# Kernel tuning notes

Hardware: AMD Instinct MI355X
Metric: run time of the kernel (lower is better)

The kernel has to match this reference:

```python
import jax, jax.numpy as jnp
import numpy as np

D, H, E = 1024, 4096, 8


def setup_inputs() -> dict:
    key = jax.random.key(0)
    ks = jax.random.split(key, 5)
    x = jax.random.normal(ks[0], (4, 2048, D), dtype=jnp.float32)
    gate_w = jax.random.normal(ks[1], (D, E), dtype=jnp.float32) * 0.02
    gate_b = jnp.zeros((E,), dtype=jnp.float32)
    w1 = jax.random.normal(ks[2], (E, D, H), dtype=jnp.float32) * 0.02
    b1 = jnp.zeros((E, H), dtype=jnp.float32)
    w2 = jax.random.normal(ks[3], (E, H, D), dtype=jnp.float32) * 0.02
    b2 = jnp.zeros((E, D), dtype=jnp.float32)
    return {"x": x, "gate_w": gate_w, "gate_b": gate_b,
            "w1": w1, "b1": b1, "w2": w2, "b2": b2, "top_k": 2}


def reference(x, gate_w, gate_b, w1, b1, w2, b2, top_k):
    orig_shape = x.shape
    xt = x.reshape(-1, x.shape[-1])                 # [T, D]
    logits = xt @ gate_w + gate_b                   # [T, E]
    probs = jax.nn.softmax(logits, axis=-1)
    topk_v, topk_i = jax.lax.top_k(probs, top_k)    # [T, k]
    T, n_exp = probs.shape
    # dense combine weights: zero for non-selected experts (same math as
    # sorted dispatch + weighted scatter-add in the original)
    comb = jnp.zeros((T, n_exp), xt.dtype).at[
        jnp.arange(T)[:, None], topk_i].set(topk_v)  # [T, E]

    def step(acc, params):
        W1, B1, W2, B2, g = params                  # g: [T]
        h = jax.nn.gelu(xt @ W1 + B1, approximate=False)  # exact erf GELU
        return acc + g[:, None] * (h @ W2 + B2), None

    out, _ = jax.lax.scan(step, jnp.zeros_like(xt),
                          (w1, b1, w2, b2, comb.T))
    return out.reshape(orig_shape)
```

## Files before the change

kernel.cpp:

```cpp
#include <hip/hip_runtime.h>
#include <hip/hip_bf16.h>


#define T_TOK 8192
#define DDIM  1024
#define HDIM  4096
#define NEXP  8

typedef __attribute__((ext_vector_type(8))) short sv8;
typedef __attribute__((ext_vector_type(4))) float fv4;

__device__ __forceinline__ float gelu_erf(float v) {
    return 0.5f * v * (1.0f + erff(v * 0.70710678118654752f));
}

__device__ __forceinline__ unsigned short f2bfbits(float f) {
    unsigned int x; __builtin_memcpy(&x, &f, 4);
    x += 0x7fffu + ((x >> 16) & 1u);
    return (unsigned short)(x >> 16);
}

__device__ __forceinline__ void split2(float f, short& h, short& l) {
    unsigned int x; __builtin_memcpy(&x, &f, 4);
    unsigned int hr = x + (0x7fffu + ((x >> 16) & 1u));
    unsigned int hbits = hr & 0xffff0000u;
    float hf; __builtin_memcpy(&hf, &hbits, 4);
    h = (short)(hr >> 16);
    l = (short)f2bfbits(f - hf);
}

__global__ __launch_bounds__(256) void zero_kernel(float* __restrict__ out,
                                                   int n, int* __restrict__ counts) {
    int i = blockIdx.x * 256 + threadIdx.x;
    if (i < n) out[i] = 0.0f;
    if (blockIdx.x == 0 && threadIdx.x < 16) counts[threadIdx.x] = 0;
}

__global__ __launch_bounds__(256) void gate_kernel(
    const float* __restrict__ x, const float* __restrict__ gw,
    const float* __restrict__ gb, int* __restrict__ counts,
    int* __restrict__ tok_idx, float* __restrict__ tok_gate) {
    const int token = blockIdx.x * 4 + (threadIdx.x >> 6);
    const int lane  = threadIdx.x & 63;
    const float* xr = x + (size_t)token * DDIM;

    float acc[8] = {0.f, 0.f, 0.f, 0.f, 0.f, 0.f, 0.f, 0.f};
    for (int d = lane; d < DDIM; d += 64) {
        const float xv = xr[d];
        const float4 g0 = *(const float4*)(gw + d * NEXP);
        const float4 g1 = *(const float4*)(gw + d * NEXP + 4);
        acc[0] = fmaf(xv, g0.x, acc[0]); acc[1] = fmaf(xv, g0.y, acc[1]);
        acc[2] = fmaf(xv, g0.z, acc[2]); acc[3] = fmaf(xv, g0.w, acc[3]);
        acc[4] = fmaf(xv, g1.x, acc[4]); acc[5] = fmaf(xv, g1.y, acc[5]);
        acc[6] = fmaf(xv, g1.z, acc[6]); acc[7] = fmaf(xv, g1.w, acc[7]);
    }
#pragma unroll
    for (int e = 0; e < 8; ++e)
        for (int off = 32; off > 0; off >>= 1)
            acc[e] += __shfl_down(acc[e], off);

    if (lane == 0) {
#pragma unroll
        for (int e = 0; e < 8; ++e) acc[e] += gb[e];
        float m = acc[0];
#pragma unroll
        for (int e = 1; e < 8; ++e) m = fmaxf(m, acc[e]);
        float p[8], s = 0.f;
#pragma unroll
        for (int e = 0; e < 8; ++e) { p[e] = expf(acc[e] - m); s += p[e]; }
        const float inv = 1.0f / s;
#pragma unroll
        for (int e = 0; e < 8; ++e) p[e] *= inv;
        int i1 = 0;
#pragma unroll
        for (int e = 1; e < 8; ++e) if (p[e] > p[i1]) i1 = e;
        int i2 = (i1 == 0) ? 1 : 0;
#pragma unroll
        for (int e = 0; e < 8; ++e) if (e != i1 && p[e] > p[i2]) i2 = e;

        int pos1 = atomicAdd(&counts[i1], 1);
        tok_idx[i1 * T_TOK + pos1]  = token;
        tok_gate[i1 * T_TOK + pos1] = p[i1];
        int pos2 = atomicAdd(&counts[i2], 1);
        tok_idx[i2 * T_TOK + pos2]  = token;
        tok_gate[i2 * T_TOK + pos2] = p[i2];
    }
}

__global__ void offs_kernel(const int* __restrict__ counts, int* __restrict__ offs) {
    if (threadIdx.x == 0 && blockIdx.x == 0) {
        int s = 0;
#pragma unroll
        for (int e = 0; e < NEXP; ++e) { offs[e] = s; s += counts[e]; }
        offs[NEXP] = s;
    }
}

__global__ __launch_bounds__(256) void ffn1_mfma(
    const float* __restrict__ x, const float* __restrict__ w1,
    const float* __restrict__ b1, const int* __restrict__ counts,
    const int* __restrict__ offs, const int* __restrict__ tok_idx,
    unsigned short* __restrict__ Hbuf) {
    const int e   = blockIdx.z;
    const int cnt = counts[e];
    const int m0  = blockIdx.y * 128;
    if (m0 >= cnt) return;
    const int n0  = blockIdx.x * 128;

    __shared__ __align__(16) short Ah[128][32], Al[128][32];
    __shared__ __align__(16) short Bh[128][32], Bl[128][32];
    __shared__ int stok[128];

    const int tid  = threadIdx.x;
    const int lane = tid & 63;
    const int wv   = tid >> 6;
    const int wr   = wv >> 1, wc = wv & 1;
    const int r16  = lane & 15, g4 = lane >> 4;

    if (tid < 128) stok[tid] = tok_idx[e * T_TOK + min(m0 + tid, cnt - 1)];
    __syncthreads();

    const float* W = w1 + (size_t)e * DDIM * HDIM;

    fv4 acc[4][4];
    const fv4 z4 = {0.f, 0.f, 0.f, 0.f};
#pragma unroll
    for (int i = 0; i < 4; ++i)
#pragma unroll
        for (int j = 0; j < 4; ++j) acc[i][j] = z4;

    for (int k0 = 0; k0 < DDIM; k0 += 32) {
#pragma unroll
        for (int h = 0; h < 2; ++h) {
            const int c   = tid + h * 256;
            const int row = c >> 2, kc = c & 3;
            const float* src = x + (size_t)stok[row] * DDIM + k0 + kc * 8;
            const float4 f0 = *(const float4*)src;
            const float4 f1 = *(const float4*)(src + 4);
            const float f[8] = {f0.x, f0.y, f0.z, f0.w, f1.x, f1.y, f1.z, f1.w};
            sv8 hv, lv;
#pragma unroll
            for (int i = 0; i < 8; ++i) { short hh, ll; split2(f[i], hh, ll); hv[i] = hh; lv[i] = ll; }
            *(sv8*)&Ah[row][kc * 8] = hv;
            *(sv8*)&Al[row][kc * 8] = lv;
        }
#pragma unroll
        for (int h = 0; h < 2; ++h) {
            const int c  = tid + h * 256;
            const int nn = c >> 2, kc = c & 3;
            float f[8];
#pragma unroll
            for (int i = 0; i < 8; ++i)
                f[i] = W[(size_t)(k0 + kc * 8 + i) * HDIM + n0 + nn];
            sv8 hv, lv;
#pragma unroll
            for (int i = 0; i < 8; ++i) { short hh, ll; split2(f[i], hh, ll); hv[i] = hh; lv[i] = ll; }
            *(sv8*)&Bh[nn][kc * 8] = hv;
            *(sv8*)&Bl[nn][kc * 8] = lv;
        }
        __syncthreads();

        sv8 a_h[4], a_l[4], b_h[4], b_l[4];
#pragma unroll
        for (int m = 0; m < 4; ++m) {
            const int row = wr * 64 + m * 16 + r16;
            a_h[m] = *(const sv8*)&Ah[row][g4 * 8];
            a_l[m] = *(const sv8*)&Al[row][g4 * 8];
        }
#pragma unroll
        for (int n = 0; n < 4; ++n) {
            const int col = wc * 64 + n * 16 + r16;
            b_h[n] = *(const sv8*)&Bh[col][g4 * 8];
            b_l[n] = *(const sv8*)&Bl[col][g4 * 8];
        }
#pragma unroll
        for (int m = 0; m < 4; ++m)
#pragma unroll
            for (int n = 0; n < 4; ++n) {
                acc[m][n] = __builtin_amdgcn_mfma_f32_16x16x32_bf16(a_h[m], b_h[n], acc[m][n], 0, 0, 0);
                acc[m][n] = __builtin_amdgcn_mfma_f32_16x16x32_bf16(a_h[m], b_l[n], acc[m][n], 0, 0, 0);
                acc[m][n] = __builtin_amdgcn_mfma_f32_16x16x32_bf16(a_l[m], b_h[n], acc[m][n], 0, 0, 0);
            }
        __syncthreads();
    }

    const int hbase = offs[e] + m0;
#pragma unroll
    for (int n = 0; n < 4; ++n) {
        const int colg = n0 + wc * 64 + n * 16 + r16;
        const float bias = b1[e * HDIM + colg];
#pragma unroll
        for (int m = 0; m < 4; ++m) {
#pragma unroll
            for (int r = 0; r < 4; ++r) {
                const int rowl = wr * 64 + m * 16 + g4 * 4 + r;
                if (m0 + rowl < cnt) {
                    const float v = gelu_erf(acc[m][n][r] + bias);
                    Hbuf[(size_t)(hbase + rowl) * HDIM + colg] = f2bfbits(v);
                }
            }
        }
    }
}

__global__ __launch_bounds__(256) void ffn2_mfma(
    const unsigned short* __restrict__ Hb, const float* __restrict__ w2,
    const float* __restrict__ b2, const int* __restrict__ counts,
    const int* __restrict__ offs, const int* __restrict__ tok_idx,
    const float* __restrict__ tok_gate, float* __restrict__ out) {
    const int e   = blockIdx.z;
    const int cnt = counts[e];
    const int m0  = blockIdx.y * 128;
    if (m0 >= cnt) return;
    const int n0  = blockIdx.x * 128;

    __shared__ __align__(16) short Ahs[128][32];
    __shared__ __align__(16) short Bh[128][32], Bl[128][32];
    __shared__ int   stok[128];
    __shared__ float sgate[128];

    const int tid  = threadIdx.x;
    const int lane = tid & 63;
    const int wv   = tid >> 6;
    const int wr   = wv >> 1, wc = wv & 1;
    const int r16  = lane & 15, g4 = lane >> 4;

    if (tid < 128) {
        const int src = e * T_TOK + min(m0 + tid, cnt - 1);
        stok[tid]  = tok_idx[src];
        sgate[tid] = tok_gate[src];
    }
    __syncthreads();

    const float* W = w2 + (size_t)e * HDIM * DDIM;
    const int oe = offs[e];

    fv4 acc[4][4];
    const fv4 z4 = {0.f, 0.f, 0.f, 0.f};
#pragma unroll
    for (int i = 0; i < 4; ++i)
#pragma unroll
        for (int j = 0; j < 4; ++j) acc[i][j] = z4;

    for (int k0 = 0; k0 < HDIM; k0 += 32) {
#pragma unroll
        for (int h = 0; h < 2; ++h) {
            const int c   = tid + h * 256;
            const int row = c >> 2, kc = c & 3;
            const size_t grow = (size_t)(oe + min(m0 + row, cnt - 1));
            *(sv8*)&Ahs[row][kc * 8] = *(const sv8*)(Hb + grow * HDIM + k0 + kc * 8);
        }
#pragma unroll
        for (int h = 0; h < 2; ++h) {
            const int c  = tid + h * 256;
            const int nn = c >> 2, kc = c & 3;
            float f[8];
#pragma unroll
            for (int i = 0; i < 8; ++i)
                f[i] = W[(size_t)(k0 + kc * 8 + i) * DDIM + n0 + nn];
            sv8 hv, lv;
#pragma unroll
            for (int i = 0; i < 8; ++i) { short hh, ll; split2(f[i], hh, ll); hv[i] = hh; lv[i] = ll; }
            *(sv8*)&Bh[nn][kc * 8] = hv;
            *(sv8*)&Bl[nn][kc * 8] = lv;
        }
        __syncthreads();

        sv8 a[4], b_h[4], b_l[4];
#pragma unroll
        for (int m = 0; m < 4; ++m) {
            const int row = wr * 64 + m * 16 + r16;
            a[m] = *(const sv8*)&Ahs[row][g4 * 8];
        }
#pragma unroll
        for (int n = 0; n < 4; ++n) {
            const int col = wc * 64 + n * 16 + r16;
            b_h[n] = *(const sv8*)&Bh[col][g4 * 8];
            b_l[n] = *(const sv8*)&Bl[col][g4 * 8];
        }
#pragma unroll
        for (int m = 0; m < 4; ++m)
#pragma unroll
            for (int n = 0; n < 4; ++n) {
                acc[m][n] = __builtin_amdgcn_mfma_f32_16x16x32_bf16(a[m], b_h[n], acc[m][n], 0, 0, 0);
                acc[m][n] = __builtin_amdgcn_mfma_f32_16x16x32_bf16(a[m], b_l[n], acc[m][n], 0, 0, 0);
            }
        __syncthreads();
    }

#pragma unroll
    for (int n = 0; n < 4; ++n) {
        const int colg = n0 + wc * 64 + n * 16 + r16;
        const float bias = b2[e * DDIM + colg];
#pragma unroll
        for (int m = 0; m < 4; ++m) {
#pragma unroll
            for (int r = 0; r < 4; ++r) {
                const int rowl = wr * 64 + m * 16 + g4 * 4 + r;
                if (m0 + rowl < cnt) {
                    const int   t  = stok[rowl];
                    const float gg = sgate[rowl];
                    atomicAdd(&out[(size_t)t * DDIM + colg], gg * (acc[m][n][r] + bias));
                }
            }
        }
    }
}

extern "C" void kernel_launch(void* const* d_in, const int* in_sizes, int n_in,
                              void* d_out, int out_size, void* d_ws, size_t ws_size,
                              hipStream_t stream) {
    const float* x      = (const float*)d_in[0];
    const float* gate_w = (const float*)d_in[1];
    const float* gate_b = (const float*)d_in[2];
    const float* w1     = (const float*)d_in[3];
    const float* b1     = (const float*)d_in[4];
    const float* w2     = (const float*)d_in[5];
    const float* b2     = (const float*)d_in[6];

    char* ws        = (char*)d_ws;
    int*   counts   = (int*)ws;
    int*   offs     = (int*)(ws + 64);
    int*   tok_idx  = (int*)(ws + 1024);
    float* tok_gate = (float*)(ws + 1024 + 262144);
    unsigned short* Hbuf = (unsigned short*)(ws + (1 << 20));

    float* out = (float*)d_out;

    zero_kernel<<<(T_TOK * DDIM + 255) / 256, 256, 0, stream>>>(out, T_TOK * DDIM, counts);
    gate_kernel<<<T_TOK / 4, 256, 0, stream>>>(x, gate_w, gate_b, counts, tok_idx, tok_gate);
    offs_kernel<<<1, 64, 0, stream>>>(counts, offs);

    dim3 g1(HDIM / 128, T_TOK / 128, NEXP);
    dim3 g2(DDIM / 128, T_TOK / 128, NEXP);
    ffn1_mfma<<<g1, 256, 0, stream>>>(x, w1, b1, counts, offs, tok_idx, Hbuf);
    ffn2_mfma<<<g2, 256, 0, stream>>>(Hbuf, w2, b2, counts, offs, tok_idx, tok_gate, out);
}
```

Baseline: 1.818 ms.

## Enlarge M tile to 256 with 512-thread blocks, pad LDS, use builtin bf16 convert

Both FFN GEMM kernels now use 512-thread blocks covering 256 token rows per tile instead of 128. Each converted weight tile is therefore reused across twice as many rows, which cuts redundant fp32 weight loads and bf16 splitting. LDS rows are padded from 32 to 40 shorts to reduce bank conflicts, and the manual bf16 rounding is replaced with the HIP intrinsic. Larger blocks raise LDS and register pressure per block, and the extra rows are wasted padding for experts with few tokens.

Result: faster. 1.532 ms (-15.7%).

```diff
diff --git a/kernel.cpp b/kernel.cpp
--- a/kernel.cpp
+++ b/kernel.cpp
@@ -14,19 +14,17 @@
     return 0.5f * v * (1.0f + erff(v * 0.70710678118654752f));
 }
 
-__device__ __forceinline__ unsigned short f2bfbits(float f) {
-    unsigned int x; __builtin_memcpy(&x, &f, 4);
-    x += 0x7fffu + ((x >> 16) & 1u);
-    return (unsigned short)(x >> 16);
+__device__ __forceinline__ short cvt_bf16(float f) {
+    __hip_bfloat16 b = __float2bfloat16(f);
+    unsigned short s; __builtin_memcpy(&s, &b, 2);
+    return (short)s;
 }
 
 __device__ __forceinline__ void split2(float f, short& h, short& l) {
-    unsigned int x; __builtin_memcpy(&x, &f, 4);
-    unsigned int hr = x + (0x7fffu + ((x >> 16) & 1u));
-    unsigned int hbits = hr & 0xffff0000u;
-    float hf; __builtin_memcpy(&hf, &hbits, 4);
-    h = (short)(hr >> 16);
-    l = (short)f2bfbits(f - hf);
+    h = cvt_bf16(f);
+    unsigned int hb = ((unsigned int)(unsigned short)h) << 16;
+    float hf; __builtin_memcpy(&hf, &hb, 4);
+    l = cvt_bf16(f - hf);
 }
 
 __global__ __launch_bounds__(256) void zero_kernel(float* __restrict__ out,
@@ -96,20 +94,20 @@
     }
 }
 
-__global__ __launch_bounds__(256) void ffn1_mfma(
+__global__ __launch_bounds__(512) void ffn1_mfma(
     const float* __restrict__ x, const float* __restrict__ w1,
     const float* __restrict__ b1, const int* __restrict__ counts,
     const int* __restrict__ offs, const int* __restrict__ tok_idx,
     unsigned short* __restrict__ Hbuf) {
     const int e   = blockIdx.z;
     const int cnt = counts[e];
-    const int m0  = blockIdx.y * 128;
+    const int m0  = blockIdx.y * 256;
     if (m0 >= cnt) return;
     const int n0  = blockIdx.x * 128;
 
-    __shared__ __align__(16) short Ah[128][32], Al[128][32];
-    __shared__ __align__(16) short Bh[128][32], Bl[128][32];
-    __shared__ int stok[128];
+    __shared__ __align__(16) short Ah[256][40], Al[256][40];
+    __shared__ __align__(16) short Bh[128][40], Bl[128][40];
+    __shared__ int stok[256];
 
     const int tid  = threadIdx.x;
     const int lane = tid & 63;
@@ -117,7 +115,7 @@
     const int wr   = wv >> 1, wc = wv & 1;
     const int r16  = lane & 15, g4 = lane >> 4;
 
-    if (tid < 128) stok[tid] = tok_idx[e * T_TOK + min(m0 + tid, cnt - 1)];
+    if (tid < 256) stok[tid] = tok_idx[e * T_TOK + min(m0 + tid, cnt - 1)];
     __syncthreads();
 
     const float* W = w1 + (size_t)e * DDIM * HDIM;
@@ -132,7 +130,7 @@
     for (int k0 = 0; k0 < DDIM; k0 += 32) {
 #pragma unroll
         for (int h = 0; h < 2; ++h) {
-            const int c   = tid + h * 256;
+            const int c   = tid + h * 512;
             const int row = c >> 2, kc = c & 3;
             const float* src = x + (size_t)stok[row] * DDIM + k0 + kc * 8;
             const float4 f0 = *(const float4*)src;
@@ -144,10 +142,8 @@
             *(sv8*)&Ah[row][kc * 8] = hv;
             *(sv8*)&Al[row][kc * 8] = lv;
         }
-#pragma unroll
-        for (int h = 0; h < 2; ++h) {
-            const int c  = tid + h * 256;
-            const int nn = c >> 2, kc = c & 3;
+        {
+            const int nn = tid >> 2, kc = tid & 3;
             float f[8];
 #pragma unroll
             for (int i = 0; i < 8; ++i)
@@ -196,28 +192,28 @@
                 const int rowl = wr * 64 + m * 16 + g4 * 4 + r;
                 if (m0 + rowl < cnt) {
                     const float v = gelu_erf(acc[m][n][r] + bias);
-                    Hbuf[(size_t)(hbase + rowl) * HDIM + colg] = f2bfbits(v);
+                    Hbuf[(size_t)(hbase + rowl) * HDIM + colg] = (unsigned short)cvt_bf16(v);
                 }
             }
         }
     }
 }
 
-__global__ __launch_bounds__(256) void ffn2_mfma(
+__global__ __launch_bounds__(512) void ffn2_mfma(
     const unsigned short* __restrict__ Hb, const float* __restrict__ w2,
     const float* __restrict__ b2, const int* __restrict__ counts,
     const int* __restrict__ offs, const int* __restrict__ tok_idx,
     const float* __restrict__ tok_gate, float* __restrict__ out) {
     const int e   = blockIdx.z;
     const int cnt = counts[e];
-    const int m0  = blockIdx.y * 128;
+    const int m0  = blockIdx.y * 256;
     if (m0 >= cnt) return;
     const int n0  = blockIdx.x * 128;
 
-    __shared__ __align__(16) short Ahs[128][32];
-    __shared__ __align__(16) short Bh[128][32], Bl[128][32];
-    __shared__ int   stok[128];
-    __shared__ float sgate[128];
+    __shared__ __align__(16) short Ahs[256][40];
+    __shared__ __align__(16) short Bh[128][40], Bl[128][40];
+    __shared__ int   stok[256];
+    __shared__ float sgate[256];
 
     const int tid  = threadIdx.x;
     const int lane = tid & 63;
@@ -225,7 +221,7 @@
     const int wr   = wv >> 1, wc = wv & 1;
     const int r16  = lane & 15, g4 = lane >> 4;
 
-    if (tid < 128) {
+    if (tid < 256) {
         const int src = e * T_TOK + min(m0 + tid, cnt - 1);
         stok[tid]  = tok_idx[src];
         sgate[tid] = tok_gate[src];
@@ -245,15 +241,13 @@
     for (int k0 = 0; k0 < HDIM; k0 += 32) {
 #pragma unroll
         for (int h = 0; h < 2; ++h) {
-            const int c   = tid + h * 256;
+            const int c   = tid + h * 512;
             const int row = c >> 2, kc = c & 3;
             const size_t grow = (size_t)(oe + min(m0 + row, cnt - 1));
             *(sv8*)&Ahs[row][kc * 8] = *(const sv8*)(Hb + grow * HDIM + k0 + kc * 8);
         }
-#pragma unroll
-        for (int h = 0; h < 2; ++h) {
-            const int c  = tid + h * 256;
-            const int nn = c >> 2, kc = c & 3;
+        {
+            const int nn = tid >> 2, kc = tid & 3;
             float f[8];
 #pragma unroll
             for (int i = 0; i < 8; ++i)
@@ -331,8 +325,8 @@
     gate_kernel<<<T_TOK / 4, 256, 0, stream>>>(x, gate_w, gate_b, counts, tok_idx, tok_gate);
     offs_kernel<<<1, 64, 0, stream>>>(counts, offs);
 
-    dim3 g1(HDIM / 128, T_TOK / 128, NEXP);
-    dim3 g2(DDIM / 128, T_TOK / 128, NEXP);
-    ffn1_mfma<<<g1, 256, 0, stream>>>(x, w1, b1, counts, offs, tok_idx, Hbuf);
-    ffn2_mfma<<<g2, 256, 0, stream>>>(Hbuf, w2, b2, counts, offs, tok_idx, tok_gate, out);
-}
+    dim3 g1(HDIM / 128, T_TOK / 256, NEXP);
+    dim3 g2(DDIM / 128, T_TOK / 256, NEXP);
+    ffn1_mfma<<<g1, 512, 0, stream>>>(x, w1, b1, counts, offs, tok_idx, Hbuf);
+    ffn2_mfma<<<g2, 512, 0, stream>>>(Hbuf, w2, b2, counts, offs, tok_idx, tok_gate, out);
+}
```
